# Performance work log

Hardware: AMD Instinct MI355X
Metric: run time of the kernel (lower is better)

## Reference

```python
import jax, jax.numpy as jnp
import numpy as np

B = 1048576
EPS = 1e-5

def _lin_params(key, din, dout):
    k1, k2 = jax.random.split(key)
    bound = 1.0 / np.sqrt(din)
    w = jax.random.uniform(k1, (din, dout), minval=-bound, maxval=bound, dtype=jnp.float32)
    b = jax.random.uniform(k2, (dout,), minval=-bound, maxval=bound, dtype=jnp.float32)
    return w, b

def setup_inputs() -> dict:
    key = jax.random.key(0)
    ks = jax.random.split(key, 10)
    x = jax.random.normal(ks[0], (B, 8), dtype=jnp.float32)
    dims = [(8, 16), (16, 16), (16, 12), (12, 8), (8, 4), (4, 4), (4, 4), (4, 1)]
    names = ['fm', 'c1', 'p1', 'c2', 'p2', 'c3', 'r', 'h']
    inp = {'x': x,
           'bn_g': jnp.ones((8,), jnp.float32),
           'bn_b': jnp.zeros((8,), jnp.float32)}
    for i, (nm, (di, do)) in enumerate(zip(names, dims)):
        w, b = _lin_params(ks[i + 1], di, do)
        inp['w_' + nm] = w
        inp['b_' + nm] = b
    return inp

def reference(x, bn_g, bn_b, w_fm, b_fm, w_c1, b_c1, w_p1, b_p1, w_c2, b_c2,
              w_p2, b_p2, w_c3, b_c3, w_r, b_r, w_h, b_h):
    # BatchNorm1d (training mode): batch statistics, biased variance
    mu = jnp.mean(x, axis=0)
    var = jnp.mean((x - mu) ** 2, axis=0)
    h = (x - mu) * jax.lax.rsqrt(var + EPS) * bn_g + bn_b
    h = jnp.tanh(h @ w_fm + b_fm)   # [B,16] feature_map
    h = jnp.tanh(h @ w_c1 + b_c1)   # [B,16] conv1
    h = jnp.tanh(h @ w_p1 + b_p1)   # [B,12] pool1
    h = jnp.tanh(h @ w_c2 + b_c2)   # [B,8]  conv2
    h = jnp.tanh(h @ w_p2 + b_p2)   # [B,4]  pool2
    h = jnp.tanh(h @ w_c3 + b_c3)   # [B,4]  conv3
    res = jax.nn.relu(h @ w_r + b_r)  # [B,4] residual branch
    h = h + res
    return jax.nn.sigmoid(h @ w_h + b_h)  # [B,1]
```

## Files before the change

### kernel.cpp

```cpp
#include <hip/hip_runtime.h>
#include <stdint.h>

#define B_ROWS 1048576
#define ROWS_PER_THREAD 2
#define MAIN_BLOCKS (B_ROWS / (256 * ROWS_PER_THREAD))

typedef __fp16 h2 __attribute__((ext_vector_type(2)));

#define WPK_OFF 16
#define BIA_OFF 386
#define W_FM 0
#define W_C1 64
#define W_P1 192
#define W_C2 288
#define W_P2 336
#define W_C3 352
#define W_R  360
#define W_H  368
#define B_FM 0
#define B_C1 16
#define B_P1 32
#define B_C2 44
#define B_P2 52
#define B_C3 56
#define B_R  60
#define B_H  64

__device__ __forceinline__ float exp_tanh(float x) {
    float e = __builtin_amdgcn_exp2f(x * 2.8853900817779268f);
    return 1.0f - 2.0f * __builtin_amdgcn_rcpf(e + 1.0f);
}

__device__ __forceinline__ float fast_sigmoid(float x) {
    float e = __builtin_amdgcn_exp2f(x * -1.4426950408889634f);
    return __builtin_amdgcn_rcpf(1.0f + e);
}

__global__ __launch_bounds__(256) void bn_stats(const float* __restrict__ x,
                                                float* __restrict__ ws) {
    const int tid = blockIdx.x * 256 + threadIdx.x;
    float s[8], q[8];
#pragma unroll
    for (int c = 0; c < 8; ++c) { s[c] = 0.f; q[c] = 0.f; }
    const float4* x4 = (const float4*)x;
#pragma unroll
    for (int k = 0; k < 4; ++k) {
        int r = tid + k * 262144;
        float4 a = x4[2 * r];
        float4 b = x4[2 * r + 1];
        s[0] += a.x; s[1] += a.y; s[2] += a.z; s[3] += a.w;
        s[4] += b.x; s[5] += b.y; s[6] += b.z; s[7] += b.w;
        q[0] += a.x * a.x; q[1] += a.y * a.y; q[2] += a.z * a.z; q[3] += a.w * a.w;
        q[4] += b.x * b.x; q[5] += b.y * b.y; q[6] += b.z * b.z; q[7] += b.w * b.w;
    }
#pragma unroll
    for (int off = 32; off > 0; off >>= 1) {
#pragma unroll
        for (int c = 0; c < 8; ++c) {
            s[c] += __shfl_down(s[c], off);
            q[c] += __shfl_down(q[c], off);
        }
    }
    __shared__ float red[4][16];
    const int lane = threadIdx.x & 63;
    const int wave = threadIdx.x >> 6;
    if (lane == 0) {
#pragma unroll
        for (int c = 0; c < 8; ++c) { red[wave][c] = s[c]; red[wave][8 + c] = q[c]; }
    }
    __syncthreads();
    if (threadIdx.x < 16) {
        float acc = red[0][threadIdx.x] + red[1][threadIdx.x] +
                    red[2][threadIdx.x] + red[3][threadIdx.x];
        atomicAdd(&ws[threadIdx.x], acc);
    }
}

template<int DIN, int DOUT>
__device__ void pack_layer(const float* __restrict__ w, const float* __restrict__ b,
                           uint32_t* __restrict__ wdst, float* __restrict__ bdst,
                           const float* sc, const float* sh, bool fold) {
    for (int idx = threadIdx.x; idx < DOUT * (DIN / 2); idx += blockDim.x) {
        int j = idx / (DIN / 2), i2 = idx % (DIN / 2);
        float w0 = w[(2 * i2) * DOUT + j];
        float w1 = w[(2 * i2 + 1) * DOUT + j];
        if (fold) { w0 *= sc[2 * i2]; w1 *= sc[2 * i2 + 1]; }
        h2 h; h.x = (__fp16)w0; h.y = (__fp16)w1;
        wdst[j * (DIN / 2) + i2] = __builtin_bit_cast(uint32_t, h);
    }
    for (int j = threadIdx.x; j < DOUT; j += blockDim.x) {
        float bb = b[j];
        if (fold) {
#pragma unroll
            for (int i = 0; i < 8; ++i) bb += sh[i] * w[i * DOUT + j];
        }
        bdst[j] = bb;
    }
}

__global__ __launch_bounds__(256) void prep(
    float* __restrict__ ws,
    const float* __restrict__ bn_g, const float* __restrict__ bn_b,
    const float* __restrict__ w_fm, const float* __restrict__ b_fm,
    const float* __restrict__ w_c1, const float* __restrict__ b_c1,
    const float* __restrict__ w_p1, const float* __restrict__ b_p1,
    const float* __restrict__ w_c2, const float* __restrict__ b_c2,
    const float* __restrict__ w_p2, const float* __restrict__ b_p2,
    const float* __restrict__ w_c3, const float* __restrict__ b_c3,
    const float* __restrict__ w_r,  const float* __restrict__ b_r,
    const float* __restrict__ w_h,  const float* __restrict__ b_h)
{
    const float invB = 1.0f / (float)B_ROWS;
    float sc[8], sh[8];
#pragma unroll
    for (int c = 0; c < 8; ++c) {
        float mu  = ws[c] * invB;
        float var = fmaf(-mu, mu, ws[8 + c] * invB);
        float s   = bn_g[c] * rsqrtf(var + 1e-5f);
        sc[c] = s;
        sh[c] = fmaf(-mu, s, bn_b[c]);
    }
    uint32_t* wpk = (uint32_t*)(ws + WPK_OFF);
    float*    bpk = ws + BIA_OFF;
    pack_layer<8, 16>(w_fm, b_fm, wpk + W_FM, bpk + B_FM, sc, sh, true);
    pack_layer<16,16>(w_c1, b_c1, wpk + W_C1, bpk + B_C1, sc, sh, false);
    pack_layer<16,12>(w_p1, b_p1, wpk + W_P1, bpk + B_P1, sc, sh, false);
    pack_layer<12, 8>(w_c2, b_c2, wpk + W_C2, bpk + B_C2, sc, sh, false);
    pack_layer<8,  4>(w_p2, b_p2, wpk + W_P2, bpk + B_P2, sc, sh, false);
    pack_layer<4,  4>(w_c3, b_c3, wpk + W_C3, bpk + B_C3, sc, sh, false);
    pack_layer<4,  4>(w_r,  b_r,  wpk + W_R,  bpk + B_R,  sc, sh, false);
    pack_layer<4,  1>(w_h,  b_h,  wpk + W_H,  bpk + B_H,  sc, sh, false);
}

__device__ __forceinline__ float lut_tanh(float x, const float2* __restrict__ lut) {
    float t  = fmaf(x, 128.0f, 512.0f);
    t = __builtin_amdgcn_fmed3f(t, 0.0f, 1023.998f);
    float fl = floorf(t);
    float fr = t - fl;
    float2 e = lut[(int)fl];
    return fmaf(e.y, fr, e.x);
}

template<int DIN, int DOUT>
__device__ __forceinline__ void layer_dot(const h2* __restrict__ apkA, const h2* __restrict__ apkB,
                                          float* __restrict__ outA, float* __restrict__ outB,
                                          const uint32_t* __restrict__ wpk,
                                          const float* __restrict__ bias) {
#pragma unroll
    for (int j = 0; j < DOUT; ++j) {
        float accA = bias[j];
        float accB = accA;
#pragma unroll
        for (int i2 = 0; i2 < DIN / 2; ++i2) {
            h2 w = __builtin_bit_cast(h2, wpk[j * (DIN / 2) + i2]);
            accA = __builtin_amdgcn_fdot2(apkA[i2], w, accA, false);
            accB = __builtin_amdgcn_fdot2(apkB[i2], w, accB, false);
        }
        outA[j] = accA;
        outB[j] = accB;
    }
}

template<int N>
__device__ __forceinline__ void tanh_pack(const float* __restrict__ inA, const float* __restrict__ inB,
                                          h2* __restrict__ pkA, h2* __restrict__ pkB,
                                          const float2* __restrict__ lut) {
#pragma unroll
    for (int k = 0; k < N / 2; ++k) {
        float a0 = lut_tanh(inA[2 * k], lut);
        float a1 = lut_tanh(inA[2 * k + 1], lut);
        float b0 = lut_tanh(inB[2 * k], lut);
        float b1 = lut_tanh(inB[2 * k + 1], lut);
        pkA[k] = __builtin_amdgcn_cvt_pkrtz(a0, a1);
        pkB[k] = __builtin_amdgcn_cvt_pkrtz(b0, b1);
    }
}

__global__ __launch_bounds__(256) void qcnn_main(
    const float* __restrict__ x,
    const float* __restrict__ ws, float* __restrict__ out)
{
    __shared__ float2 lut[1024];
    {
        const float h = 0.0078125f;
#pragma unroll
        for (int k = 0; k < 4; ++k) {
            int i = threadIdx.x + k * 256;
            float x0 = fmaf((float)i, h, -4.0f);
            float t0 = exp_tanh(x0);
            float t1 = exp_tanh(x0 + h);
            lut[i] = make_float2(t0, t1 - t0);
        }
    }
    __syncthreads();

    const uint32_t* wpk = (const uint32_t*)(ws + WPK_OFF);
    const float*    bpk = ws + BIA_OFF;

    const int tid = blockIdx.x * 256 + threadIdx.x;
    const int r0 = tid, r1 = tid + (B_ROWS / 2);
    const float4* x4 = (const float4*)x;
    float4 xa0 = x4[2 * r0], xa1 = x4[2 * r0 + 1];
    float4 xb0 = x4[2 * r1], xb1 = x4[2 * r1 + 1];

    h2 a8[4], b8[4];
    a8[0] = __builtin_amdgcn_cvt_pkrtz(xa0.x, xa0.y);
    a8[1] = __builtin_amdgcn_cvt_pkrtz(xa0.z, xa0.w);
    a8[2] = __builtin_amdgcn_cvt_pkrtz(xa1.x, xa1.y);
    a8[3] = __builtin_amdgcn_cvt_pkrtz(xa1.z, xa1.w);
    b8[0] = __builtin_amdgcn_cvt_pkrtz(xb0.x, xb0.y);
    b8[1] = __builtin_amdgcn_cvt_pkrtz(xb0.z, xb0.w);
    b8[2] = __builtin_amdgcn_cvt_pkrtz(xb1.x, xb1.y);
    b8[3] = __builtin_amdgcn_cvt_pkrtz(xb1.z, xb1.w);

    float oA[16], oB[16]; h2 pA[8], pB[8];
    layer_dot<8, 16>(a8, b8, oA, oB, wpk + W_FM, bpk + B_FM);
    tanh_pack<16>(oA, oB, pA, pB, lut);
    float o2A[16], o2B[16]; h2 p2A[8], p2B[8];
    layer_dot<16,16>(pA, pB, o2A, o2B, wpk + W_C1, bpk + B_C1);
    tanh_pack<16>(o2A, o2B, p2A, p2B, lut);
    float o3A[12], o3B[12]; h2 p3A[6], p3B[6];
    layer_dot<16,12>(p2A, p2B, o3A, o3B, wpk + W_P1, bpk + B_P1);
    tanh_pack<12>(o3A, o3B, p3A, p3B, lut);
    float o4A[8], o4B[8]; h2 p4A[4], p4B[4];
    layer_dot<12, 8>(p3A, p3B, o4A, o4B, wpk + W_C2, bpk + B_C2);
    tanh_pack<8>(o4A, o4B, p4A, p4B, lut);
    float o5A[4], o5B[4]; h2 p5A[2], p5B[2];
    layer_dot<8,  4>(p4A, p4B, o5A, o5B, wpk + W_P2, bpk + B_P2);
    tanh_pack<4>(o5A, o5B, p5A, p5B, lut);
    float c4A[4], c4B[4];
    layer_dot<4,  4>(p5A, p5B, c4A, c4B, wpk + W_C3, bpk + B_C3);
#pragma unroll
    for (int j = 0; j < 4; ++j) {
        c4A[j] = lut_tanh(c4A[j], lut);
        c4B[j] = lut_tanh(c4B[j], lut);
    }
    h2 pcA[2], pcB[2];
    pcA[0] = __builtin_amdgcn_cvt_pkrtz(c4A[0], c4A[1]);
    pcA[1] = __builtin_amdgcn_cvt_pkrtz(c4A[2], c4A[3]);
    pcB[0] = __builtin_amdgcn_cvt_pkrtz(c4B[0], c4B[1]);
    pcB[1] = __builtin_amdgcn_cvt_pkrtz(c4B[2], c4B[3]);
    float r4A[4], r4B[4];
    layer_dot<4,  4>(pcA, pcB, r4A, r4B, wpk + W_R, bpk + B_R);
#pragma unroll
    for (int j = 0; j < 4; ++j) {
        c4A[j] += fmaxf(r4A[j], 0.f);
        c4B[j] += fmaxf(r4B[j], 0.f);
    }
    h2 phA[2], phB[2];
    phA[0] = __builtin_amdgcn_cvt_pkrtz(c4A[0], c4A[1]);
    phA[1] = __builtin_amdgcn_cvt_pkrtz(c4A[2], c4A[3]);
    phB[0] = __builtin_amdgcn_cvt_pkrtz(c4B[0], c4B[1]);
    phB[1] = __builtin_amdgcn_cvt_pkrtz(c4B[2], c4B[3]);
    float ohA[1], ohB[1];
    layer_dot<4,  1>(phA, phB, ohA, ohB, wpk + W_H, bpk + B_H);
    out[r0] = fast_sigmoid(ohA[0]);
    out[r1] = fast_sigmoid(ohB[0]);
}

extern "C" void kernel_launch(void* const* d_in, const int* in_sizes, int n_in,
                              void* d_out, int out_size, void* d_ws, size_t ws_size,
                              hipStream_t stream) {
    const float* x    = (const float*)d_in[0];
    const float* bn_g = (const float*)d_in[1];
    const float* bn_b = (const float*)d_in[2];
    const float* w_fm = (const float*)d_in[3];
    const float* b_fm = (const float*)d_in[4];
    const float* w_c1 = (const float*)d_in[5];
    const float* b_c1 = (const float*)d_in[6];
    const float* w_p1 = (const float*)d_in[7];
    const float* b_p1 = (const float*)d_in[8];
    const float* w_c2 = (const float*)d_in[9];
    const float* b_c2 = (const float*)d_in[10];
    const float* w_p2 = (const float*)d_in[11];
    const float* b_p2 = (const float*)d_in[12];
    const float* w_c3 = (const float*)d_in[13];
    const float* b_c3 = (const float*)d_in[14];
    const float* w_r  = (const float*)d_in[15];
    const float* b_r  = (const float*)d_in[16];
    const float* w_h  = (const float*)d_in[17];
    const float* b_h  = (const float*)d_in[18];
    float* out = (float*)d_out;
    float* ws  = (float*)d_ws;

    (void)hipMemsetAsync(d_ws, 0, 16 * sizeof(float), stream);
    bn_stats<<<1024, 256, 0, stream>>>(x, ws);
    prep<<<1, 256, 0, stream>>>(ws, bn_g, bn_b, w_fm, b_fm, w_c1, b_c1, w_p1, b_p1,
                                w_c2, b_c2, w_p2, b_p2, w_c3, b_c3, w_r, b_r, w_h, b_h);
    qcnn_main<<<MAIN_BLOCKS, 256, 0, stream>>>(x, ws, out);
}
```

Baseline: 153.3 us.

## Replace atomic BN stat accumulation with per-block partials reduced in prep

Each bn_stats block now writes its 16 partial sums to its own slot in the workspace instead of issuing atomicAdds, and the prep kernel reduces the 1024 partials in shared memory. This removes the hipMemsetAsync launch and the atomic contention on 16 addresses. The workspace layout shifts to make room for the partials. The x loads in the main kernel are also hoisted above the LUT construction so global memory latency overlaps the table build.

After: 146.6 us. 4.4% less time.

```diff
diff --git a/kernel.cpp b/kernel.cpp
--- a/kernel.cpp
+++ b/kernel.cpp
@@ -4,11 +4,13 @@
 #define B_ROWS 1048576
 #define ROWS_PER_THREAD 2
 #define MAIN_BLOCKS (B_ROWS / (256 * ROWS_PER_THREAD))
+#define STAT_BLOCKS 1024
 
 typedef __fp16 h2 __attribute__((ext_vector_type(2)));
 
-#define WPK_OFF 16
-#define BIA_OFF 386
+#define PART_OFF 16
+#define WPK_OFF 16400
+#define BIA_OFF 16770
 #define W_FM 0
 #define W_C1 64
 #define W_P1 192
@@ -72,7 +74,7 @@
     if (threadIdx.x < 16) {
         float acc = red[0][threadIdx.x] + red[1][threadIdx.x] +
                     red[2][threadIdx.x] + red[3][threadIdx.x];
-        atomicAdd(&ws[threadIdx.x], acc);
+        ws[PART_OFF + blockIdx.x * 16 + threadIdx.x] = acc;
     }
 }
 
@@ -110,26 +112,45 @@
     const float* __restrict__ w_r,  const float* __restrict__ b_r,
     const float* __restrict__ w_h,  const float* __restrict__ b_h)
 {
-    const float invB = 1.0f / (float)B_ROWS;
-    float sc[8], sh[8];
-#pragma unroll
-    for (int c = 0; c < 8; ++c) {
-        float mu  = ws[c] * invB;
-        float var = fmaf(-mu, mu, ws[8 + c] * invB);
+    __shared__ float acc[16][17];
+    __shared__ float scs[8], shs[8];
+    {
+        const int f = threadIdx.x & 15;
+        const int chunk = threadIdx.x >> 4;
+        float a = 0.f;
+        const float* p = ws + PART_OFF + (chunk * 64) * 16 + f;
+#pragma unroll 8
+        for (int b = 0; b < 64; ++b) a += p[b * 16];
+        acc[chunk][f] = a;
+    }
+    __syncthreads();
+    if (threadIdx.x < 16) {
+        float t = 0.f;
+#pragma unroll
+        for (int c = 0; c < 16; ++c) t += acc[c][threadIdx.x];
+        acc[16 - 16][threadIdx.x] = t;
+    }
+    __syncthreads();
+    if (threadIdx.x < 8) {
+        const float invB = 1.0f / (float)B_ROWS;
+        int c = threadIdx.x;
+        float mu  = acc[0][c] * invB;
+        float var = fmaf(-mu, mu, acc[0][8 + c] * invB);
         float s   = bn_g[c] * rsqrtf(var + 1e-5f);
-        sc[c] = s;
-        sh[c] = fmaf(-mu, s, bn_b[c]);
-    }
+        scs[c] = s;
+        shs[c] = fmaf(-mu, s, bn_b[c]);
+    }
+    __syncthreads();
     uint32_t* wpk = (uint32_t*)(ws + WPK_OFF);
     float*    bpk = ws + BIA_OFF;
-    pack_layer<8, 16>(w_fm, b_fm, wpk + W_FM, bpk + B_FM, sc, sh, true);
-    pack_layer<16,16>(w_c1, b_c1, wpk + W_C1, bpk + B_C1, sc, sh, false);
-    pack_layer<16,12>(w_p1, b_p1, wpk + W_P1, bpk + B_P1, sc, sh, false);
-    pack_layer<12, 8>(w_c2, b_c2, wpk + W_C2, bpk + B_C2, sc, sh, false);
-    pack_layer<8,  4>(w_p2, b_p2, wpk + W_P2, bpk + B_P2, sc, sh, false);
-    pack_layer<4,  4>(w_c3, b_c3, wpk + W_C3, bpk + B_C3, sc, sh, false);
-    pack_layer<4,  4>(w_r,  b_r,  wpk + W_R,  bpk + B_R,  sc, sh, false);
-    pack_layer<4,  1>(w_h,  b_h,  wpk + W_H,  bpk + B_H,  sc, sh, false);
+    pack_layer<8, 16>(w_fm, b_fm, wpk + W_FM, bpk + B_FM, scs, shs, true);
+    pack_layer<16,16>(w_c1, b_c1, wpk + W_C1, bpk + B_C1, scs, shs, false);
+    pack_layer<16,12>(w_p1, b_p1, wpk + W_P1, bpk + B_P1, scs, shs, false);
+    pack_layer<12, 8>(w_c2, b_c2, wpk + W_C2, bpk + B_C2, scs, shs, false);
+    pack_layer<8,  4>(w_p2, b_p2, wpk + W_P2, bpk + B_P2, scs, shs, false);
+    pack_layer<4,  4>(w_c3, b_c3, wpk + W_C3, bpk + B_C3, scs, shs, false);
+    pack_layer<4,  4>(w_r,  b_r,  wpk + W_R,  bpk + B_R,  scs, shs, false);
+    pack_layer<4,  1>(w_h,  b_h,  wpk + W_H,  bpk + B_H,  scs, shs, false);
 }
 
 __device__ __forceinline__ float lut_tanh(float x, const float2* __restrict__ lut) {
@@ -180,6 +201,12 @@
     const float* __restrict__ x,
     const float* __restrict__ ws, float* __restrict__ out)
 {
+    const int tid = blockIdx.x * 256 + threadIdx.x;
+    const int r0 = tid, r1 = tid + (B_ROWS / 2);
+    const float4* x4 = (const float4*)x;
+    float4 xa0 = x4[2 * r0], xa1 = x4[2 * r0 + 1];
+    float4 xb0 = x4[2 * r1], xb1 = x4[2 * r1 + 1];
+
     __shared__ float2 lut[1024];
     {
         const float h = 0.0078125f;
@@ -196,12 +223,6 @@
 
     const uint32_t* wpk = (const uint32_t*)(ws + WPK_OFF);
     const float*    bpk = ws + BIA_OFF;
-
-    const int tid = blockIdx.x * 256 + threadIdx.x;
-    const int r0 = tid, r1 = tid + (B_ROWS / 2);
-    const float4* x4 = (const float4*)x;
-    float4 xa0 = x4[2 * r0], xa1 = x4[2 * r0 + 1];
-    float4 xb0 = x4[2 * r1], xb1 = x4[2 * r1 + 1];
 
     h2 a8[4], b8[4];
     a8[0] = __builtin_amdgcn_cvt_pkrtz(xa0.x, xa0.y);
@@ -283,8 +304,7 @@
     float* out = (float*)d_out;
     float* ws  = (float*)d_ws;
 
-    (void)hipMemsetAsync(d_ws, 0, 16 * sizeof(float), stream);
-    bn_stats<<<1024, 256, 0, stream>>>(x, ws);
+    bn_stats<<<STAT_BLOCKS, 256, 0, stream>>>(x, ws);
     prep<<<1, 256, 0, stream>>>(ws, bn_g, bn_b, w_fm, b_fm, w_c1, b_c1, w_p1, b_p1,
                                 w_c2, b_c2, w_p2, b_p2, w_c3, b_c3, w_r, b_r, w_h, b_h);
     qcnn_main<<<MAIN_BLOCKS, 256, 0, stream>>>(x, ws, out);
```
